# Performance work log

Hardware: AMD Instinct MI355X
Metric: run time of the kernel (lower is better)

Reference implementation:

```python
import jax, jax.numpy as jnp
import numpy as np

B, S, H, W = 1, 4, 224, 224
NUM_SAMPLES = 4096
DEPTH_MIN = 1e-6
POSE_W, DEPTH_W, POINTS_W, NORMAL_W = 1.0, 1.0, 1.0, 1.0
EPS = 1e-6


def setup_inputs():
    key = jax.random.key(0)
    k1, k2, k3, k4, k5 = jax.random.split(key, 5)
    depth_pred = jax.random.uniform(k1, (B, S, H, W), jnp.float32) * 5.0 + 0.1
    depth_gt = jax.random.uniform(k2, (B, S, H, W), jnp.float32) * 5.0 + 0.05
    points_pred = jax.random.normal(k3, (B, S, H, W, 3), jnp.float32)
    intr = jnp.array([[200.0, 0.0, W / 2.0], [0.0, 200.0, H / 2.0], [0.0, 0.0, 1.0]], jnp.float32)
    intrinsics = jnp.broadcast_to(intr, (B, S, 3, 3))
    pose_gt = jnp.broadcast_to(jnp.eye(4, dtype=jnp.float32), (B, S, 4, 4))
    pose_gt = pose_gt.at[..., :3, 3].set(jax.random.normal(k4, (B, S, 3), jnp.float32) * 0.1)
    pose_pred = pose_gt.at[..., :3, 3].add(jax.random.normal(k5, (B, S, 3), jnp.float32) * 0.01)
    return {"depth_pred": depth_pred, "points_pred": points_pred, "depth_gt": depth_gt,
            "intrinsics": intrinsics, "pose_pred": pose_pred, "pose_gt": pose_gt}


def _cam_points(depth, intrinsics):
    # depth [B,S,H,W] -> camera-frame points [B,S,H,W,3] (unprojection)
    h, w = depth.shape[-2:]
    ys, xs = jnp.meshgrid(jnp.arange(h, dtype=depth.dtype), jnp.arange(w, dtype=depth.dtype), indexing="ij")
    fx = jnp.maximum(intrinsics[..., 0, 0], EPS)[..., None, None]
    fy = jnp.maximum(intrinsics[..., 1, 1], EPS)[..., None, None]
    cx = intrinsics[..., 0, 2][..., None, None]
    cy = intrinsics[..., 1, 2][..., None, None]
    x = (xs - cx) / fx * depth
    y = (ys - cy) / fy * depth
    return jnp.stack([x, y, depth], axis=-1)


def _depth_to_normals(depth, intrinsics):
    pts = _cam_points(depth, intrinsics)
    fx_diff = pts[..., 1:-1, 2:, :] - pts[..., 1:-1, :-2, :]
    fy_diff = pts[..., 2:, 1:-1, :] - pts[..., :-2, 1:-1, :]
    core = jnp.cross(fy_diff, fx_diff, axis=-1)
    core = core / jnp.maximum(jnp.linalg.norm(core, axis=-1, keepdims=True), EPS)
    return jnp.zeros_like(pts).at[..., 1:-1, 1:-1, :].set(core)


def _depth_to_world(depth, intrinsics, pose):
    pts = _cam_points(depth, intrinsics)
    rot, trans = pose[..., :3, :3], pose[..., :3, 3]
    return jnp.einsum("bsij,bshwj->bshwi", rot, pts) + trans[:, :, None, None, :]


def _relative_to_first(c2w):
    return jnp.linalg.inv(c2w[:, 0:1]) @ c2w


def _align_depth_scale(depth_pred, depth_gt, mask):
    # per-(b,s) median-ratio scale on detached prediction, as in align_depth_scale
    dp = jax.lax.stop_gradient(depth_pred)
    m = mask & jnp.isfinite(dp) & (dp > EPS)
    ratio = jnp.where(m, dp / jnp.maximum(depth_gt, EPS), jnp.nan)
    med = jnp.nanmedian(ratio.reshape(ratio.shape[0], ratio.shape[1], -1), axis=-1)
    cnt = m.reshape(m.shape[0], m.shape[1], -1).sum(-1)
    scale = jnp.where((cnt < 16) | ~jnp.isfinite(med), 1.0, jnp.clip(med, 1e-3, 1e3))
    return depth_gt * scale[..., None, None], scale


def _masked_l1(pred, target, mask):
    w = mask.astype(pred.dtype)
    return (jnp.abs(pred - target) * w).sum() / jnp.maximum(w.sum(), 1.0)


def _masked_cosine(pred, target, mask):
    pn = pred / jnp.maximum(jnp.linalg.norm(pred, axis=-1, keepdims=True), EPS)
    tn = target / jnp.maximum(jnp.linalg.norm(target, axis=-1, keepdims=True), EPS)
    cos = jnp.clip((pn * tn).sum(-1), -1.0, 1.0)
    w = mask.astype(pred.dtype)
    return ((1.0 - cos) * w).sum() / jnp.maximum(w.sum(), 1.0)


def _masked_chamfer(pred_pts, gt_pts, mask):
    # pred_pts/gt_pts [N,H,W,3], mask [N,H,W]; per-frame masked subsample + chamfer
    n = pred_pts.shape[0]
    pf = pred_pts.reshape(n, -1, 3)
    gf = gt_pts.reshape(n, -1, 3)
    mf = mask.reshape(n, -1)
    hw = pf.shape[1]
    idx = jnp.arange(hw, dtype=jnp.uint32)
    # deterministic pseudo-random jitter (Knuth hash) stands in for randperm subsampling
    jitter = ((idx * jnp.uint32(2654435761)) % jnp.uint32(1 << 20)).astype(jnp.float32) / float(1 << 20)

    def frame(p, g, m):
        score = m.astype(jnp.float32) * 2.0 + jitter
        _, sel = jax.lax.top_k(score, NUM_SAMPLES)
        ps, gs, ms = p[sel], g[sel], m[sel]
        d2 = jnp.sum(ps * ps, -1)[:, None] + jnp.sum(gs * gs, -1)[None, :] - 2.0 * (ps @ gs.T)
        d = jnp.sqrt(jnp.maximum(d2, 1e-12))  # [NUM_SAMPLES, NUM_SAMPLES]
        big = jnp.asarray(1e9, d.dtype)
        min_pg = jnp.min(jnp.where(ms[None, :], d, big), axis=1)
        min_gp = jnp.min(jnp.where(ms[:, None], d, big), axis=0)
        w = ms.astype(d.dtype)
        denom = jnp.maximum(w.sum(), 1.0)
        cd = (min_pg * w).sum() / denom + (min_gp * w).sum() / denom
        ok = m.sum() >= 10
        return jnp.where(ok, cd, 0.0), ok.astype(d.dtype)

    cds, oks = jax.vmap(frame)(pf, gf, mf)
    return cds.sum() / jnp.maximum(oks.sum(), 1.0)


def reference(depth_pred, points_pred, depth_gt, intrinsics, pose_pred, pose_gt):
    mask = (depth_gt > 0) & jnp.isfinite(depth_gt) & (depth_gt > DEPTH_MIN)
    depth_gt_al, _ = _align_depth_scale(depth_pred, depth_gt, mask)
    rel_pred = _relative_to_first(pose_pred)
    rel_gt = _relative_to_first(pose_gt)
    pose_loss = jnp.mean(jnp.abs(rel_pred - rel_gt))
    depth_loss = _masked_l1(depth_pred, depth_gt_al, mask)
    points_gt = _depth_to_world(depth_gt_al, intrinsics, rel_gt)
    b, s, h, w = depth_gt.shape
    points_loss = _masked_chamfer(points_pred.reshape(b * s, h, w, 3),
                                  points_gt.reshape(b * s, h, w, 3),
                                  mask.reshape(b * s, h, w))
    normal_loss = _masked_cosine(_depth_to_normals(depth_pred, intrinsics),
                                 _depth_to_normals(depth_gt_al, intrinsics), mask)
    return POSE_W * pose_loss + DEPTH_W * depth_loss + POINTS_W * points_loss + NORMAL_W * normal_loss
```

## Files before the change

kernel.cpp:

```cpp
#include <hip/hip_runtime.h>
#include <stdint.h>

#define HW   50176
#define IMW  224
#define NS   4096
#define EPSF 1e-6f
#define NRB  16384
#define NKB  2048

#define OFF_PS   256
#define OFF_HIST 256
#define OFF_KH   65792
#define OFF_SEL  65792
#define OFF_GS   82176
#define OFF_RMIN 147712

__device__ __forceinline__ bool finitef(float x){
  return (__float_as_uint(x) & 0x7f800000u) != 0x7f800000u;
}
__device__ __forceinline__ uint32_t ordenc(float f){
  uint32_t u = __float_as_uint(f);
  return (u & 0x80000000u) ? ~u : (u | 0x80000000u);
}
__device__ __forceinline__ float orddec(uint32_t e){
  uint32_t u = (e & 0x80000000u) ? (e & 0x7fffffffu) : ~e;
  return __uint_as_float(u);
}
__device__ __forceinline__ int wsum_i(int v){
  #pragma unroll
  for (int o=32;o;o>>=1) v += __shfl_down(v,o);
  return v;
}
__device__ __forceinline__ float wsum_f(float v){
  #pragma unroll
  for (int o=32;o;o>>=1) v += __shfl_down(v,o);
  return v;
}
__device__ __forceinline__ int block_prefix_incl(int v, int* lds){
  int tid = threadIdx.x;
  lds[tid] = v; __syncthreads();
  #pragma unroll
  for (int off=1; off<256; off<<=1){
    int add = (tid>=off) ? lds[tid-off] : 0;
    __syncthreads();
    lds[tid] += add;
    __syncthreads();
  }
  return lds[tid];
}

__device__ void inv4(const float* A, float* out){
  float M[4][8];
  for (int i=0;i<4;i++) for (int j=0;j<4;j++){ M[i][j]=A[i*4+j]; M[i][4+j]=(i==j)?1.f:0.f; }
  for (int c=0;c<4;c++){
    int piv=c; float mx=fabsf(M[c][c]);
    for (int r=c+1;r<4;r++){ float a=fabsf(M[r][c]); if (a>mx){ mx=a; piv=r; } }
    if (piv!=c) for (int j=0;j<8;j++){ float t=M[c][j]; M[c][j]=M[piv][j]; M[piv][j]=t; }
    float inv = 1.f/M[c][c];
    for (int j=0;j<8;j++) M[c][j]*=inv;
    for (int r=0;r<4;r++){
      if (r==c) continue;
      float fv = M[r][c];
      for (int j=0;j<8;j++) M[r][j] -= fv*M[c][j];
    }
  }
  for (int i=0;i<4;i++) for (int j=0;j<4;j++) out[i*4+j]=M[i][4+j];
}
__device__ void mat4(const float* A, const float* B, float* C){
  for (int i=0;i<4;i++) for (int j=0;j<4;j++){
    float s=0.f;
    for (int k=0;k<4;k++) s += A[i*4+k]*B[k*4+j];
    C[i*4+j]=s;
  }
}
__device__ __forceinline__ float3 normal_at(const float* D, float sc, int x, int y,
                                            float cx, float cy, float fx, float fy){
  int base = y*IMW + x;
  float dL = D[base-1]*sc,   dR = D[base+1]*sc;
  float dU = D[base-IMW]*sc, dD = D[base+IMW]*sc;
  float xl = ((float)(x-1)-cx)/fx, xr = ((float)(x+1)-cx)/fx, xc = ((float)x-cx)/fx;
  float yu = ((float)(y-1)-cy)/fy, yd = ((float)(y+1)-cy)/fy, yc = ((float)y-cy)/fy;
  float ax = xc*dD - xc*dU, ay = yd*dD - yu*dU, az = dD - dU;
  float bx = xr*dR - xl*dL, by = yc*dR - yc*dL, bz = dR - dL;
  float nx = ay*bz - az*by;
  float ny = az*bx - ax*bz;
  float nz = ax*by - ay*bx;
  float l = sqrtf(nx*nx + ny*ny + nz*nz);
  float inv = 1.f/fmaxf(l, EPSF);
  return make_float3(nx*inv, ny*inv, nz*inv);
}

__global__ __launch_bounds__(256) void k_zero(float* W){
  int gid = blockIdx.x*256 + threadIdx.x;
  if (gid < 18496) ((float4*)W)[gid] = make_float4(0.f,0.f,0.f,0.f);
}

__global__ __launch_bounds__(1024) void k_hist(const float* dp_, const float* dg_,
                                               const float* pp, const float* pg, float* W){
  const int bid = blockIdx.x, tid = threadIdx.x;
  if (bid == 32){
    if (tid != 0) return;
    float i0p[16], i0g[16];
    inv4(pp, i0p); inv4(pg, i0g);
    float s = 0.f;
    for (int f=0; f<4; f++){
      float rp[16], rg[16];
      mat4(i0p, pp+16*f, rp);
      mat4(i0g, pg+16*f, rg);
      for (int k=0;k<16;k++) s += fabsf(rp[k]-rg[k]);
      for (int i=0;i<3;i++) for (int j=0;j<3;j++) W[72+f*12+i*3+j] = rg[i*4+j];
      for (int i=0;i<3;i++) W[72+f*12+9+i] = rg[i*4+3];
    }
    W[0] = s/64.f;
    return;
  }
  __shared__ uint32_t lh[NRB + NKB];
  for (int j=tid; j<NRB+NKB; j+=1024) lh[j] = 0u;
  __syncthreads();
  const int f = bid >> 3;
  const int base = (bid & 7) * 6272;
  int nn_l = 0, mc_l = 0;
  #pragma unroll
  for (int it=0; it<2; ++it){
    int t = tid + it*1024;
    if (t < 1568){
      float4 d4 = *(const float4*)(dg_ + f*HW + base + t*4);
      float4 p4 = *(const float4*)(dp_ + f*HW + base + t*4);
      float dv[4] = {d4.x,d4.y,d4.z,d4.w};
      float pv[4] = {p4.x,p4.y,p4.z,p4.w};
      #pragma unroll
      for (int k=0;k<4;++k){
        int r = base + t*4 + k;
        bool mg = (dv[k] > EPSF) && finitef(dv[k]);
        bool m  = mg && finitef(pv[k]) && (pv[k] > EPSF);
        mc_l += mg ? 1 : 0;
        nn_l += m ? 1 : 0;
        if (m){
          uint32_t u = __float_as_uint(pv[k] / fmaxf(dv[k], EPSF));
          atomicAdd(&lh[u>>18], 1u);
        }
        uint32_t key = ((uint32_t)(mg?1:0) << 20) | (((uint32_t)r*2654435761u) & 0xFFFFFu);
        atomicAdd(&lh[NRB + (key>>10)], 1u);
      }
    }
  }
  __syncthreads();
  uint32_t* HIST  = (uint32_t*)(W + OFF_HIST) + f*NRB;
  uint32_t* KHIST = (uint32_t*)(W + OFF_KH)   + f*NKB;
  for (int j=tid; j<NRB; j+=1024){ uint32_t v = lh[j]; if (v) atomicAdd(&HIST[j], v); }
  for (int j=tid; j<NKB; j+=1024){ uint32_t v = lh[NRB+j]; if (v) atomicAdd(&KHIST[j], v); }
  int* I = (int*)(W + 24);
  int nw = wsum_i(nn_l), mw = wsum_i(mc_l);
  if ((tid & 63) == 0){ atomicAdd(&I[4+f], nw); atomicAdd(&I[8+f], mw); }
}

__global__ __launch_bounds__(256) void k_scan(float* W){
  const int f = blockIdx.x, tid = threadIdx.x;
  __shared__ int slds[256];
  int* I = (int*)(W + 24);
  const uint32_t* FH = (const uint32_t*)(W + OFF_HIST) + f*NRB;
  int part = 0;
  for (int j=0;j<64;j++) part += (int)FH[tid*64+j];
  int incl = block_prefix_incl(part, slds);
  int nn = I[4+f];
  if (nn > 0){
    int k1 = (nn-1)>>1, k2 = nn>>1;
    int acc = incl - part;
    for (int j=0;j<64;j++){
      int c = (int)FH[tid*64+j];
      if (k1 >= acc && k1 < acc+c){ I[20+f] = tid*64+j; I[24+f] = k1-acc; }
      if (k2 >= acc && k2 < acc+c){ I[28+f] = tid*64+j; I[32+f] = k2-acc; }
      acc += c;
    }
  } else if (tid == 0){ I[20+f] = -1; I[28+f] = -1; }
  __syncthreads();
  const uint32_t* FK = (const uint32_t*)(W + OFF_KH) + f*NKB;
  int kpart = 0;
  int kl[8];
  #pragma unroll
  for (int j=0;j<8;j++){ kl[j] = (int)FK[tid*8+j]; kpart += kl[j]; }
  int kincl = block_prefix_incl(kpart, slds);
  {
    const int tt = HW - NS;
    int acc = kincl - kpart;
    #pragma unroll
    for (int j=0;j<8;j++){
      if (tt >= acc && tt < acc+kl[j]){ I[36+f] = tid*8+j; I[40+f] = tt-acc; }
      acc += kl[j];
    }
  }
}

__global__ __launch_bounds__(256) void k_collect(const float* dp_, const float* dg_, float* W){
  __shared__ int slds[256];
  __shared__ int base_s, base_c;
  const int bid = blockIdx.x, tid = threadIdx.x;
  const int f = bid / 49;
  const int base = (bid - f*49)*1024;
  int* I = (int*)(W + 24);
  uint32_t* CAND  = (uint32_t*)(W + OFF_RMIN);
  uint32_t* KCAND = CAND + 16384;
  int* SEL = (int*)(W + OFF_SEL);
  const int b1 = I[20+f], b2 = I[28+f], bk = I[36+f];
  float4 d4 = *(const float4*)(dg_ + f*HW + base + tid*4);
  float4 p4 = *(const float4*)(dp_ + f*HW + base + tid*4);
  float dv[4] = {d4.x,d4.y,d4.z,d4.w};
  float pv[4] = {p4.x,p4.y,p4.z,p4.w};
  bool sf[4], cf[4];
  uint32_t cu[4];
  int cnt_s = 0, cnt_c = 0;
  #pragma unroll
  for (int k=0;k<4;++k){
    int r = base + tid*4 + k;
    bool mg = (dv[k] > EPSF) && finitef(dv[k]);
    bool m  = mg && finitef(pv[k]) && (pv[k] > EPSF);
    cu[k] = 0u; cf[k] = false;
    if (m){
      cu[k] = __float_as_uint(pv[k] / fmaxf(dv[k], EPSF));
      int bu = (int)(cu[k]>>18);
      cf[k] = (bu == b1 || bu == b2);
    }
    uint32_t key = ((uint32_t)(mg?1:0) << 20) | (((uint32_t)r*2654435761u) & 0xFFFFFu);
    int kb = (int)(key>>10);
    sf[k] = kb > bk;
    cnt_s += sf[k] ? 1 : 0;
    cnt_c += cf[k] ? 1 : 0;
    if (kb == bk){
      int p = atomicAdd(&I[16+f], 1);
      if (p < 4096) KCAND[f*4096 + p] = (uint32_t)r;
    }
  }
  int packed = (cnt_c<<11) | cnt_s;
  int incl = block_prefix_incl(packed, slds);
  int excl = incl - packed;
  int excl_s = excl & 0x7FF, excl_c = excl >> 11;
  int tot = slds[255];
  if (tid == 0){
    base_s = atomicAdd(&I[0+f],  tot & 0x7FF);
    base_c = atomicAdd(&I[12+f], tot >> 11);
  }
  __syncthreads();
  int ps = base_s + excl_s, pc = base_c + excl_c;
  #pragma unroll
  for (int k=0;k<4;++k){
    int r = base + tid*4 + k;
    if (sf[k]) SEL[(f<<12) + ps++] = r;
    if (cf[k]){ if (pc < 4096) CAND[f*4096 + pc] = cu[k]; pc++; }
  }
}

__device__ uint32_t refine_rank(const uint32_t* sC, int nc, uint32_t b, int r,
                                int* hist, int* slds){
  const int tid = threadIdx.x;
  __shared__ int ssb, srem;
  hist[tid] = 0; __syncthreads();
  for (int t=tid; t<nc; t+=256){
    uint32_t c = sC[t];
    if ((c>>18) == b) atomicAdd(&hist[(c>>10)&0xFF], 1);
  }
  __syncthreads();
  int part = hist[tid];
  int incl = block_prefix_incl(part, slds);
  if (part > 0 && r >= incl-part && r < incl){ ssb = tid; srem = r-(incl-part); }
  __syncthreads();
  uint32_t pfx = (b<<8) | (uint32_t)ssb;
  int r2 = srem;
  __syncthreads();
  hist[tid] = 0; __syncthreads();
  for (int t=tid; t<nc; t+=256){
    uint32_t c = sC[t];
    if ((c>>10) == pfx) atomicAdd(&hist[(c>>2)&0xFF], 1);
  }
  __syncthreads();
  part = hist[tid];
  incl = block_prefix_incl(part, slds);
  if (part > 0 && r2 >= incl-part && r2 < incl){ ssb = tid; srem = r2-(incl-part); }
  __syncthreads();
  uint32_t pfx2 = (pfx<<8) | (uint32_t)ssb;
  int r3 = srem;
  __syncthreads();
  if (tid < 4) hist[tid] = 0;
  __syncthreads();
  for (int t=tid; t<nc; t+=256){
    uint32_t c = sC[t];
    if ((c>>2) == pfx2) atomicAdd(&hist[c&3], 1);
  }
  __syncthreads();
  int h0=hist[0], h1=hist[1], h2=hist[2];
  uint32_t lo = (r3 < h0) ? 0u : (r3 < h0+h1) ? 1u : (r3 < h0+h1+h2) ? 2u : 3u;
  __syncthreads();
  return (pfx2<<2) | lo;
}

__global__ __launch_bounds__(256) void k_finish(const float* dg_, const float* pts_,
                                                const float* intr, float* W){
  const int f = blockIdx.x, tid = threadIdx.x;
  __shared__ __align__(16) uint32_t smem[8192];
  __shared__ int hist[256];
  __shared__ int slds[256];
  int* I = (int*)(W + 24);
  uint32_t* CAND  = (uint32_t*)(W + OFF_RMIN);
  uint32_t* KCAND = CAND + 16384;
  int* SEL = (int*)(W + OFF_SEL);
  uint32_t* sC = smem;
  uint32_t* sK = smem + 4096;
  int nc = min(I[12+f], 4096), nk = min(I[16+f], 4096);
  for (int t=tid; t<nc; t+=256) sC[t] = CAND[f*4096 + t];
  for (int t=tid; t<nk; t+=256) sK[t] = KCAND[f*4096 + t];
  __syncthreads();
  for (int t=tid; t<4096; t+=256){
    CAND [f*4096 + t] = 0xFF800000u;
    KCAND[f*4096 + t] = 0xFF800000u;
  }
  int nn = I[4+f], mc = I[8+f];
  float scale = 1.f;
  if (nn > 0){
    uint32_t v1 = refine_rank(sC, nc, (uint32_t)I[20+f], I[24+f], hist, slds);
    uint32_t v2 = refine_rank(sC, nc, (uint32_t)I[28+f], I[32+f], hist, slds);
    float med = 0.5f*(__uint_as_float(v1) + __uint_as_float(v2));
    scale = (nn < 16 || !finitef(med)) ? 1.f : fminf(fmaxf(med, 1e-3f), 1e3f);
  }
  {
    int bk = I[36+f], rk = I[40+f];
    uint32_t maskbit = ((uint32_t)bk >> 10) & 1u;
    for (int t=tid; t<nk; t+=256){
      uint32_t i = sK[t];
      uint32_t key = (maskbit<<20) | ((i*2654435761u) & 0xFFFFFu);
      int rank = 0;
      for (int j=0;j<nk;j++){
        uint32_t key2 = (maskbit<<20) | ((sK[j]*2654435761u) & 0xFFFFFu);
        rank += (key2 < key);
      }
      if (rank >= rk){ int p = atomicAdd(&I[0+f], 1); SEL[(f<<12)+p] = (int)i; }
    }
  }
  __syncthreads();
  if (tid == 0){ W[20+f] = scale; W[16+f] = (float)mc; }
  float fx = fmaxf(intr[f*9+0], EPSF), fy = fmaxf(intr[f*9+4], EPSF);
  float cx = intr[f*9+2], cy = intr[f*9+5];
  const float* R = W + 72 + f*12;
  float wl = 0.f;
  for (int t=tid; t<4096; t+=256){
    int idx = SEL[(f<<12)+t];
    float dgv = dg_[f*HW + idx];
    bool mg = (dgv > EPSF) && finitef(dgv);
    float wv = mg ? 1.f : 0.f;
    wl += wv;
    const float* p = pts_ + (size_t)(f*HW + idx)*3;
    ((float4*)(W + OFF_PS))[(f<<12)+t] = make_float4(p[0], p[1], p[2], wv);
    float d = dgv * scale;
    int y = idx / IMW, x = idx - y*IMW;
    float X = ((float)x - cx)/fx * d;
    float Y = ((float)y - cy)/fy * d;
    float4 gs;
    gs.x = R[0]*X + R[1]*Y + R[2]*d + R[9];
    gs.y = R[3]*X + R[4]*Y + R[5]*d + R[10];
    gs.z = R[6]*X + R[7]*Y + R[8]*d + R[11];
    gs.w = wv;
    ((float4*)(W + OFF_GS))[(f<<12)+t] = gs;
  }
  float ws = wsum_f(wl);
  if ((tid & 63) == 0) atomicAdd(&W[12+f], ws);
}

__global__ __launch_bounds__(256) void k_cham(const float* dp_, const float* dg_,
                                              const float* intr, float* W){
  __shared__ __align__(16) float4 tile[256];
  __shared__ float rsum[8];
  const int bid = blockIdx.x, tid = threadIdx.x;
  {
    int dir = bid >> 8;
    int rem = bid & 255;
    int f = rem >> 6;
    int t64 = rem & 63;
    int rc = t64 & 3;
    int gc = t64 >> 2;
    const float4* PS = (const float4*)(W + OFF_PS);
    const float4* GS = (const float4*)(W + OFF_GS);
    const float4* A = dir ? GS : PS;
    const float4* B = dir ? PS : GS;
    uint32_t* RM = (uint32_t*)(W + OFF_RMIN) + dir*16384 + (f<<12);
    {
      float4 b = B[(f<<12) + (gc<<8) + tid];
      float gg = fmaf(b.x,b.x, fmaf(b.y,b.y, b.z*b.z));
      bool v = b.w > 0.f;
      tile[tid] = make_float4(v?b.x:0.f, v?b.y:0.f, v?b.z:0.f, v ? -0.5f*gg : -INFINITY);
    }
    __syncthreads();
    int r0 = (rc<<10) + tid;
    float4 a0 = A[(f<<12)+r0];
    float4 a1 = A[(f<<12)+r0+256];
    float4 a2 = A[(f<<12)+r0+512];
    float4 a3 = A[(f<<12)+r0+768];
    float rh0 = -0.5f*fmaf(a0.x,a0.x,fmaf(a0.y,a0.y,a0.z*a0.z));
    float rh1 = -0.5f*fmaf(a1.x,a1.x,fmaf(a1.y,a1.y,a1.z*a1.z));
    float rh2 = -0.5f*fmaf(a2.x,a2.x,fmaf(a2.y,a2.y,a2.z*a2.z));
    float rh3 = -0.5f*fmaf(a3.x,a3.x,fmaf(a3.y,a3.y,a3.z*a3.z));
    float m0 = -INFINITY, m1 = -INFINITY, m2 = -INFINITY, m3 = -INFINITY;
    #pragma unroll 8
    for (int j=0;j<256;++j){
      float4 g = tile[j];
      float d0 = fmaf(a0.z,g.z, fmaf(a0.y,g.y, fmaf(a0.x,g.x, rh0)));
      float d1 = fmaf(a1.z,g.z, fmaf(a1.y,g.y, fmaf(a1.x,g.x, rh1)));
      float d2 = fmaf(a2.z,g.z, fmaf(a2.y,g.y, fmaf(a2.x,g.x, rh2)));
      float d3 = fmaf(a3.z,g.z, fmaf(a3.y,g.y, fmaf(a3.x,g.x, rh3)));
      m0 = fmaxf(m0, d0 + g.w);
      m1 = fmaxf(m1, d1 + g.w);
      m2 = fmaxf(m2, d2 + g.w);
      m3 = fmaxf(m3, d3 + g.w);
    }
    atomicMin(&RM[r0    ], ordenc(-2.f*m0));
    atomicMin(&RM[r0+256], ordenc(-2.f*m1));
    atomicMin(&RM[r0+512], ordenc(-2.f*m2));
    atomicMin(&RM[r0+768], ordenc(-2.f*m3));
  }
  {
    int f = bid >> 7;
    int base = (bid & 127) * 392;
    float sc = W[20+f];
    float fx = fmaxf(intr[f*9+0], EPSF), fy = fmaxf(intr[f*9+4], EPSF);
    float cx = intr[f*9+2], cy = intr[f*9+5];
    float dl = 0.f, nl = 0.f;
    #pragma unroll
    for (int it=0; it<2; ++it){
      int t = tid + it*256;
      if (t < 392){
        int r = base + t;
        int y = r / IMW, x = r - y*IMW;
        float dgv = dg_[f*HW+r], dpv = dp_[f*HW+r];
        bool mg = (dgv > EPSF) && finitef(dgv);
        float mv = mg ? 1.f : 0.f;
        dl += fabsf(dpv - dgv*sc) * mv;
        if (x > 0 && x < IMW-1 && y > 0 && y < IMW-1){
          float3 n1 = normal_at(dp_ + f*HW, 1.f, x, y, cx, cy, fx, fy);
          float3 n2 = normal_at(dg_ + f*HW, sc,  x, y, cx, cy, fx, fy);
          float l1 = sqrtf(n1.x*n1.x + n1.y*n1.y + n1.z*n1.z);
          float l2 = sqrtf(n2.x*n2.x + n2.y*n2.y + n2.z*n2.z);
          float i1 = 1.f/fmaxf(l1, EPSF), i2 = 1.f/fmaxf(l2, EPSF);
          float cosv = (n1.x*n2.x + n1.y*n2.y + n1.z*n2.z)*i1*i2;
          cosv = fminf(fmaxf(cosv, -1.f), 1.f);
          nl += (1.f - cosv) * mv;
        } else {
          nl += mv;
        }
      }
    }
    float ds = wsum_f(dl), ns2 = wsum_f(nl);
    if ((tid & 63) == 0){ rsum[tid>>6] = ds; rsum[4+(tid>>6)] = ns2; }
    __syncthreads();
    if (tid == 0){
      atomicAdd(&W[1], rsum[0]+rsum[1]+rsum[2]+rsum[3]);
      atomicAdd(&W[3], rsum[4]+rsum[5]+rsum[6]+rsum[7]);
    }
  }
}

__global__ __launch_bounds__(1024) void k_final(float* W, float* out){
  __shared__ float flds[16];
  const int tid = threadIdx.x;
  const uint32_t* RM = (const uint32_t*)(W + OFF_RMIN);
  float sums[8];
  #pragma unroll
  for (int grp=0; grp<8; ++grp){
    int dir = grp >> 2, f = grp & 3;
    const float4* A = dir ? (const float4*)(W + OFF_GS) : (const float4*)(W + OFF_PS);
    float local = 0.f;
    for (int row=tid; row<4096; row+=1024){
      float val = orddec(RM[dir*16384 + (f<<12) + row]);
      float d = isinf(val) ? 1e9f : sqrtf(fmaxf(val, 1e-12f));
      local += d * A[(f<<12)+row].w;
    }
    local = wsum_f(local);
    __syncthreads();
    if ((tid & 63) == 0) flds[tid>>6] = local;
    __syncthreads();
    float s = 0.f;
    if (tid == 0){ for (int k=0;k<16;k++) s += flds[k]; }
    sums[grp] = s;
    __syncthreads();
  }
  if (tid == 0){
    float md = fmaxf(W[16]+W[17]+W[18]+W[19], 1.f);
    float depth_loss  = W[1]/md;
    float normal_loss = W[3]/md;
    float cds = 0.f, oks = 0.f;
    for (int f=0; f<4; f++){
      if (W[16+f] >= 10.f){
        float denom = fmaxf(W[12+f], 1.f);
        cds += sums[f]/denom + sums[4+f]/denom;
        oks += 1.f;
      }
    }
    float points_loss = cds / fmaxf(oks, 1.f);
    out[0] = W[0] + depth_loss + points_loss + normal_loss;
  }
}

extern "C" void kernel_launch(void* const* d_in, const int* in_sizes, int n_in,
                              void* d_out, int out_size, void* d_ws, size_t ws_size,
                              hipStream_t stream){
  const float* depth_pred  = (const float*)d_in[0];
  const float* points_pred = (const float*)d_in[1];
  const float* depth_gt    = (const float*)d_in[2];
  const float* intr        = (const float*)d_in[3];
  const float* pose_pred   = (const float*)d_in[4];
  const float* pose_gt     = (const float*)d_in[5];
  float* out = (float*)d_out;
  float* W   = (float*)d_ws;

  k_zero   <<<73,  256,  0, stream>>>(W);
  k_hist   <<<33,  1024, 0, stream>>>(depth_pred, depth_gt, pose_pred, pose_gt, W);
  k_scan   <<<4,   256,  0, stream>>>(W);
  k_collect<<<196, 256,  0, stream>>>(depth_pred, depth_gt, W);
  k_finish <<<4,   256,  0, stream>>>(depth_gt, points_pred, intr, W);
  k_cham   <<<512, 256,  0, stream>>>(depth_pred, depth_gt, intr, W);
  k_final  <<<1,   1024, 0, stream>>>(W, out);
}
```

Baseline: 177.2 us.

## Fold scan and final reduction into preceding kernels via last-block-done pattern

Removes the separate k_scan and k_final launches. A global atomic counter lets the last finishing block of k_hist run the histogram prefix scans and median/threshold selection for all four frames, and the last block of k_cham run the final chamfer reduction and loss assembly. This targets per-launch overhead and the idle gaps between small dependent kernels. In exchange, the scan for the four frames now runs serially in one 1024-thread block instead of four parallel blocks, and the final reduction uses 256 threads instead of 1024, adding threadfences and a serialized tail.

```diff
diff --git a/kernel.cpp b/kernel.cpp
--- a/kernel.cpp
+++ b/kernel.cpp
@@ -41,6 +41,18 @@
   lds[tid] = v; __syncthreads();
   #pragma unroll
   for (int off=1; off<256; off<<=1){
+    int add = (tid>=off) ? lds[tid-off] : 0;
+    __syncthreads();
+    lds[tid] += add;
+    __syncthreads();
+  }
+  return lds[tid];
+}
+__device__ __forceinline__ int block_prefix_incl_1024(int v, int* lds){
+  int tid = threadIdx.x;
+  lds[tid] = v; __syncthreads();
+  #pragma unroll
+  for (int off=1; off<1024; off<<=1){
     int add = (tid>=off) ? lds[tid-off] : 0;
     __syncthreads();
     lds[tid] += add;
@@ -98,96 +110,101 @@
 __global__ __launch_bounds__(1024) void k_hist(const float* dp_, const float* dg_,
                                                const float* pp, const float* pg, float* W){
   const int bid = blockIdx.x, tid = threadIdx.x;
+  __shared__ uint32_t lh[NRB + NKB];
+  int* I = (int*)(W + 24);
   if (bid == 32){
-    if (tid != 0) return;
-    float i0p[16], i0g[16];
-    inv4(pp, i0p); inv4(pg, i0g);
-    float s = 0.f;
-    for (int f=0; f<4; f++){
-      float rp[16], rg[16];
-      mat4(i0p, pp+16*f, rp);
-      mat4(i0g, pg+16*f, rg);
-      for (int k=0;k<16;k++) s += fabsf(rp[k]-rg[k]);
-      for (int i=0;i<3;i++) for (int j=0;j<3;j++) W[72+f*12+i*3+j] = rg[i*4+j];
-      for (int i=0;i<3;i++) W[72+f*12+9+i] = rg[i*4+3];
-    }
-    W[0] = s/64.f;
-    return;
-  }
-  __shared__ uint32_t lh[NRB + NKB];
-  for (int j=tid; j<NRB+NKB; j+=1024) lh[j] = 0u;
-  __syncthreads();
-  const int f = bid >> 3;
-  const int base = (bid & 7) * 6272;
-  int nn_l = 0, mc_l = 0;
-  #pragma unroll
-  for (int it=0; it<2; ++it){
-    int t = tid + it*1024;
-    if (t < 1568){
-      float4 d4 = *(const float4*)(dg_ + f*HW + base + t*4);
-      float4 p4 = *(const float4*)(dp_ + f*HW + base + t*4);
-      float dv[4] = {d4.x,d4.y,d4.z,d4.w};
-      float pv[4] = {p4.x,p4.y,p4.z,p4.w};
+    if (tid == 0){
+      float i0p[16], i0g[16];
+      inv4(pp, i0p); inv4(pg, i0g);
+      float s = 0.f;
+      for (int f=0; f<4; f++){
+        float rp[16], rg[16];
+        mat4(i0p, pp+16*f, rp);
+        mat4(i0g, pg+16*f, rg);
+        for (int k=0;k<16;k++) s += fabsf(rp[k]-rg[k]);
+        for (int i=0;i<3;i++) for (int j=0;j<3;j++) W[72+f*12+i*3+j] = rg[i*4+j];
+        for (int i=0;i<3;i++) W[72+f*12+9+i] = rg[i*4+3];
+      }
+      W[0] = s/64.f;
+    }
+  } else {
+    for (int j=tid; j<NRB+NKB; j+=1024) lh[j] = 0u;
+    __syncthreads();
+    const int f = bid >> 3;
+    const int base = (bid & 7) * 6272;
+    int nn_l = 0, mc_l = 0;
+    #pragma unroll
+    for (int it=0; it<2; ++it){
+      int t = tid + it*1024;
+      if (t < 1568){
+        float4 d4 = *(const float4*)(dg_ + f*HW + base + t*4);
+        float4 p4 = *(const float4*)(dp_ + f*HW + base + t*4);
+        float dv[4] = {d4.x,d4.y,d4.z,d4.w};
+        float pv[4] = {p4.x,p4.y,p4.z,p4.w};
+        #pragma unroll
+        for (int k=0;k<4;++k){
+          int r = base + t*4 + k;
+          bool mg = (dv[k] > EPSF) && finitef(dv[k]);
+          bool m  = mg && finitef(pv[k]) && (pv[k] > EPSF);
+          mc_l += mg ? 1 : 0;
+          nn_l += m ? 1 : 0;
+          if (m){
+            uint32_t u = __float_as_uint(pv[k] / fmaxf(dv[k], EPSF));
+            atomicAdd(&lh[u>>18], 1u);
+          }
+          uint32_t key = ((uint32_t)(mg?1:0) << 20) | (((uint32_t)r*2654435761u) & 0xFFFFFu);
+          atomicAdd(&lh[NRB + (key>>10)], 1u);
+        }
+      }
+    }
+    __syncthreads();
+    uint32_t* HIST  = (uint32_t*)(W + OFF_HIST) + f*NRB;
+    uint32_t* KHIST = (uint32_t*)(W + OFF_KH)   + f*NKB;
+    for (int j=tid; j<NRB; j+=1024){ uint32_t v = lh[j]; if (v) atomicAdd(&HIST[j], v); }
+    for (int j=tid; j<NKB; j+=1024){ uint32_t v = lh[NRB+j]; if (v) atomicAdd(&KHIST[j], v); }
+    int nw = wsum_i(nn_l), mw = wsum_i(mc_l);
+    if ((tid & 63) == 0){ atomicAdd(&I[4+f], nw); atomicAdd(&I[8+f], mw); }
+  }
+  __syncthreads();
+  __shared__ int win;
+  if (tid == 0){
+    __threadfence();
+    win = (atomicAdd((int*)(W+125), 1) == 32) ? 1 : 0;
+  }
+  __syncthreads();
+  if (!win) return;
+  __threadfence();
+  int* pls = (int*)lh;
+  for (int f=0; f<4; ++f){
+    const uint32_t* FH = (const uint32_t*)(W + OFF_HIST) + f*NRB;
+    int loc[16], part = 0;
+    #pragma unroll
+    for (int j=0;j<16;j++){ loc[j] = (int)FH[tid*16+j]; part += loc[j]; }
+    int incl = block_prefix_incl_1024(part, pls);
+    int nn = I[4+f];
+    if (nn > 0){
+      int k1 = (nn-1)>>1, k2 = nn>>1;
+      int acc = incl - part;
       #pragma unroll
-      for (int k=0;k<4;++k){
-        int r = base + t*4 + k;
-        bool mg = (dv[k] > EPSF) && finitef(dv[k]);
-        bool m  = mg && finitef(pv[k]) && (pv[k] > EPSF);
-        mc_l += mg ? 1 : 0;
-        nn_l += m ? 1 : 0;
-        if (m){
-          uint32_t u = __float_as_uint(pv[k] / fmaxf(dv[k], EPSF));
-          atomicAdd(&lh[u>>18], 1u);
-        }
-        uint32_t key = ((uint32_t)(mg?1:0) << 20) | (((uint32_t)r*2654435761u) & 0xFFFFFu);
-        atomicAdd(&lh[NRB + (key>>10)], 1u);
-      }
-    }
-  }
-  __syncthreads();
-  uint32_t* HIST  = (uint32_t*)(W + OFF_HIST) + f*NRB;
-  uint32_t* KHIST = (uint32_t*)(W + OFF_KH)   + f*NKB;
-  for (int j=tid; j<NRB; j+=1024){ uint32_t v = lh[j]; if (v) atomicAdd(&HIST[j], v); }
-  for (int j=tid; j<NKB; j+=1024){ uint32_t v = lh[NRB+j]; if (v) atomicAdd(&KHIST[j], v); }
-  int* I = (int*)(W + 24);
-  int nw = wsum_i(nn_l), mw = wsum_i(mc_l);
-  if ((tid & 63) == 0){ atomicAdd(&I[4+f], nw); atomicAdd(&I[8+f], mw); }
-}
-
-__global__ __launch_bounds__(256) void k_scan(float* W){
-  const int f = blockIdx.x, tid = threadIdx.x;
-  __shared__ int slds[256];
-  int* I = (int*)(W + 24);
-  const uint32_t* FH = (const uint32_t*)(W + OFF_HIST) + f*NRB;
-  int part = 0;
-  for (int j=0;j<64;j++) part += (int)FH[tid*64+j];
-  int incl = block_prefix_incl(part, slds);
-  int nn = I[4+f];
-  if (nn > 0){
-    int k1 = (nn-1)>>1, k2 = nn>>1;
-    int acc = incl - part;
-    for (int j=0;j<64;j++){
-      int c = (int)FH[tid*64+j];
-      if (k1 >= acc && k1 < acc+c){ I[20+f] = tid*64+j; I[24+f] = k1-acc; }
-      if (k2 >= acc && k2 < acc+c){ I[28+f] = tid*64+j; I[32+f] = k2-acc; }
-      acc += c;
-    }
-  } else if (tid == 0){ I[20+f] = -1; I[28+f] = -1; }
-  __syncthreads();
-  const uint32_t* FK = (const uint32_t*)(W + OFF_KH) + f*NKB;
-  int kpart = 0;
-  int kl[8];
-  #pragma unroll
-  for (int j=0;j<8;j++){ kl[j] = (int)FK[tid*8+j]; kpart += kl[j]; }
-  int kincl = block_prefix_incl(kpart, slds);
-  {
-    const int tt = HW - NS;
-    int acc = kincl - kpart;
-    #pragma unroll
-    for (int j=0;j<8;j++){
-      if (tt >= acc && tt < acc+kl[j]){ I[36+f] = tid*8+j; I[40+f] = tt-acc; }
-      acc += kl[j];
-    }
+      for (int j=0;j<16;j++){
+        int c = loc[j];
+        if (k1 >= acc && k1 < acc+c){ I[20+f] = tid*16+j; I[24+f] = k1-acc; }
+        if (k2 >= acc && k2 < acc+c){ I[28+f] = tid*16+j; I[32+f] = k2-acc; }
+        acc += c;
+      }
+    } else if (tid == 0){ I[20+f] = -1; I[28+f] = -1; }
+    __syncthreads();
+    const uint32_t* FK = (const uint32_t*)(W + OFF_KH) + f*NKB;
+    int l0 = (int)FK[tid*2], l1 = (int)FK[tid*2+1];
+    int kincl = block_prefix_incl_1024(l0+l1, pls);
+    {
+      const int tt = HW - NS;
+      int acc = kincl - (l0+l1);
+      if (tt >= acc && tt < acc+l0){ I[36+f] = tid*2;   I[40+f] = tt-acc; }
+      acc += l0;
+      if (tt >= acc && tt < acc+l1){ I[36+f] = tid*2+1; I[40+f] = tt-acc; }
+    }
+    __syncthreads();
   }
 }
 
@@ -364,10 +381,12 @@
 }
 
 __global__ __launch_bounds__(256) void k_cham(const float* dp_, const float* dg_,
-                                              const float* intr, float* W){
+                                              const float* intr, float* W, float* out){
   __shared__ __align__(16) float4 tile[256];
   __shared__ float rsum[8];
   const int bid = blockIdx.x, tid = threadIdx.x;
+  const float4* PS = (const float4*)(W + OFF_PS);
+  const float4* GS = (const float4*)(W + OFF_GS);
   {
     int dir = bid >> 8;
     int rem = bid & 255;
@@ -375,8 +394,6 @@
     int t64 = rem & 63;
     int rc = t64 & 3;
     int gc = t64 >> 2;
-    const float4* PS = (const float4*)(W + OFF_PS);
-    const float4* GS = (const float4*)(W + OFF_GS);
     const float4* A = dir ? GS : PS;
     const float4* B = dir ? PS : GS;
     uint32_t* RM = (uint32_t*)(W + OFF_RMIN) + dir*16384 + (f<<12);
@@ -453,46 +470,52 @@
       atomicAdd(&W[3], rsum[4]+rsum[5]+rsum[6]+rsum[7]);
     }
   }
-}
-
-__global__ __launch_bounds__(1024) void k_final(float* W, float* out){
-  __shared__ float flds[16];
-  const int tid = threadIdx.x;
-  const uint32_t* RM = (const uint32_t*)(W + OFF_RMIN);
-  float sums[8];
-  #pragma unroll
-  for (int grp=0; grp<8; ++grp){
-    int dir = grp >> 2, f = grp & 3;
-    const float4* A = dir ? (const float4*)(W + OFF_GS) : (const float4*)(W + OFF_PS);
-    float local = 0.f;
-    for (int row=tid; row<4096; row+=1024){
-      float val = orddec(RM[dir*16384 + (f<<12) + row]);
-      float d = isinf(val) ? 1e9f : sqrtf(fmaxf(val, 1e-12f));
-      local += d * A[(f<<12)+row].w;
-    }
-    local = wsum_f(local);
-    __syncthreads();
-    if ((tid & 63) == 0) flds[tid>>6] = local;
-    __syncthreads();
-    float s = 0.f;
-    if (tid == 0){ for (int k=0;k<16;k++) s += flds[k]; }
-    sums[grp] = s;
-    __syncthreads();
-  }
+  __syncthreads();
+  __shared__ int win;
   if (tid == 0){
-    float md = fmaxf(W[16]+W[17]+W[18]+W[19], 1.f);
-    float depth_loss  = W[1]/md;
-    float normal_loss = W[3]/md;
-    float cds = 0.f, oks = 0.f;
-    for (int f=0; f<4; f++){
-      if (W[16+f] >= 10.f){
-        float denom = fmaxf(W[12+f], 1.f);
-        cds += sums[f]/denom + sums[4+f]/denom;
-        oks += 1.f;
-      }
-    }
-    float points_loss = cds / fmaxf(oks, 1.f);
-    out[0] = W[0] + depth_loss + points_loss + normal_loss;
+    __threadfence();
+    win = (atomicAdd((int*)(W+126), 1) == 511) ? 1 : 0;
+  }
+  __syncthreads();
+  if (!win) return;
+  __threadfence();
+  {
+    const uint32_t* RM = (const uint32_t*)(W + OFF_RMIN);
+    float sums[8];
+    #pragma unroll
+    for (int grp=0; grp<8; ++grp){
+      int dir = grp >> 2, f = grp & 3;
+      const float4* A = dir ? GS : PS;
+      float local = 0.f;
+      for (int row=tid; row<4096; row+=256){
+        float val = orddec(RM[dir*16384 + (f<<12) + row]);
+        float d = isinf(val) ? 1e9f : sqrtf(fmaxf(val, 1e-12f));
+        local += d * A[(f<<12)+row].w;
+      }
+      local = wsum_f(local);
+      __syncthreads();
+      if ((tid & 63) == 0) rsum[tid>>6] = local;
+      __syncthreads();
+      float s = 0.f;
+      if (tid == 0){ for (int k=0;k<4;k++) s += rsum[k]; }
+      sums[grp] = s;
+      __syncthreads();
+    }
+    if (tid == 0){
+      float md = fmaxf(W[16]+W[17]+W[18]+W[19], 1.f);
+      float depth_loss  = W[1]/md;
+      float normal_loss = W[3]/md;
+      float cds = 0.f, oks = 0.f;
+      for (int f=0; f<4; f++){
+        if (W[16+f] >= 10.f){
+          float denom = fmaxf(W[12+f], 1.f);
+          cds += sums[f]/denom + sums[4+f]/denom;
+          oks += 1.f;
+        }
+      }
+      float points_loss = cds / fmaxf(oks, 1.f);
+      out[0] = W[0] + depth_loss + points_loss + normal_loss;
+    }
   }
 }
 
@@ -510,9 +533,7 @@
 
   k_zero   <<<73,  256,  0, stream>>>(W);
   k_hist   <<<33,  1024, 0, stream>>>(depth_pred, depth_gt, pose_pred, pose_gt, W);
-  k_scan   <<<4,   256,  0, stream>>>(W);
   k_collect<<<196, 256,  0, stream>>>(depth_pred, depth_gt, W);
   k_finish <<<4,   256,  0, stream>>>(depth_gt, points_pred, intr, W);
-  k_cham   <<<512, 256,  0, stream>>>(depth_pred, depth_gt, intr, W);
-  k_final  <<<1,   1024, 0, stream>>>(W, out);
-}
+  k_cham   <<<512, 256,  0, stream>>>(depth_pred, depth_gt, intr, W, out);
+}
```

Result: slower. 220.0 us (+24.1%).
